# Optimization experiments

Measured on AMD Instinct MI355X. Metric: run time of the kernel, lower is better.

The kernel has to match this reference:

```python
import jax, jax.numpy as jnp
import numpy as np

B, N, E = 16, 4096, 65536
IN, H = 256, 512
G1, G2 = 32, 32
M1, M2 = 1024, 32768
GOD = 8
BN_EPS = 1e-5


def setup_inputs() -> dict:
    key = jax.random.key(0)
    ks = jax.random.split(key, 16)
    rn = lambda i, sh, s=0.05: jax.random.normal(ks[i], sh, dtype=jnp.float32) * s
    return {
        "x": jax.random.normal(ks[0], (B, IN), dtype=jnp.float32),
        "smoothed_vert_pos": jax.random.normal(ks[1], (B, N * 3), dtype=jnp.float32),
        "hidden": jnp.zeros((B, H), jnp.float32),
        "edge_index": jax.random.randint(ks[2], (2, E), 0, N),
        "W0": rn(3, (G1, 3), 0.3), "a0_src": rn(4, (G1,), 0.3), "a0_dst": rn(5, (G1,), 0.3), "b0": jnp.zeros((G1,), jnp.float32),
        "W1": rn(6, (G2, G1), 0.2), "a1_src": rn(7, (G2,), 0.2), "a1_dst": rn(8, (G2,), 0.2), "b1": jnp.zeros((G2,), jnp.float32),
        "w_ih": rn(9, (3 * H, IN)), "w_hh": rn(10, (3 * H, H)),
        "b_ih": jnp.zeros((3 * H,), jnp.float32), "b_hh": jnp.zeros((3 * H,), jnp.float32),
        "lin1_w": rn(11, (M1, H)), "lin1_b": jnp.zeros((M1,), jnp.float32),
        "prelu1": jnp.full((M1,), 0.25, jnp.float32), "bn1_g": jnp.ones((M1,), jnp.float32), "bn1_b": jnp.zeros((M1,), jnp.float32),
        "lin2_w": rn(12, (M2, M1), 0.02), "lin2_b": jnp.zeros((M2,), jnp.float32),
        "prelu2": jnp.full((M2,), 0.25, jnp.float32), "bn2_g": jnp.ones((M2,), jnp.float32), "bn2_b": jnp.zeros((M2,), jnp.float32),
        "w_out": rn(13, (3, G2 + GOD), 0.2), "b_out": jnp.zeros((3,), jnp.float32),
    }


def _gat(v, src, dst, W, a_s, a_d, b):
    # PyG GATConv, heads=1, eval mode (no dropout), self-loops already in src/dst
    h = v @ W.T                                           # [N, F]
    e = jax.nn.leaky_relu((h * a_s).sum(-1)[src] + (h * a_d).sum(-1)[dst], 0.2)  # [E+N]
    m = jax.ops.segment_max(e, dst, num_segments=N)       # segment-softmax over incoming edges
    w = jnp.exp(e - m[dst])
    s = jax.ops.segment_sum(w, dst, num_segments=N)
    coef = w / s[dst]
    return jax.ops.segment_sum(coef[:, None] * h[src], dst, num_segments=N) + b


def _mlp_layer(t, w, bb, p, g, be):
    t = t @ w.T + bb                                      # Linear
    t = jnp.where(t >= 0, t, p * t)                       # PReLU (per-channel)
    # eval BatchNorm1d with running_mean=0, running_var=1
    return (t / jnp.sqrt(1.0 + BN_EPS)) * g + be


def reference(x, smoothed_vert_pos, hidden, edge_index,
              W0, a0_src, a0_dst, b0, W1, a1_src, a1_dst, b1,
              w_ih, w_hh, b_ih, b_hh,
              lin1_w, lin1_b, prelu1, bn1_g, bn1_b,
              lin2_w, lin2_b, prelu2, bn2_g, bn2_b,
              w_out, b_out):
    sv = smoothed_vert_pos.reshape(B, N, 3)
    loop = jnp.arange(N, dtype=edge_index.dtype)
    src = jnp.concatenate([edge_index[0], loop])          # GATConv add_self_loops=True
    dst = jnp.concatenate([edge_index[1], loop])
    gat0 = jax.vmap(lambda v: _gat(v, src, dst, W0, a0_src, a0_dst, b0))(sv)   # [B,N,G1]
    gat1 = jax.vmap(lambda v: _gat(v, src, dst, W1, a1_src, a1_dst, b1))(gat0)  # [B,N,G2]

    # GRUCell
    gi = x @ w_ih.T + b_ih
    gh = hidden @ w_hh.T + b_hh
    ir, iz, inn = jnp.split(gi, 3, axis=-1)
    hr, hz, hn = jnp.split(gh, 3, axis=-1)
    r = jax.nn.sigmoid(ir + hr)
    z = jax.nn.sigmoid(iz + hz)
    n = jnp.tanh(inn + r * hn)
    next_hidden = (1.0 - z) * n + z * hidden              # [B,H]

    o = _mlp_layer(next_hidden, lin1_w, lin1_b, prelu1, bn1_g, bn1_b)
    o = _mlp_layer(o, lin2_w, lin2_b, prelu2, bn2_g, bn2_b)
    gru_out = o.reshape(B, N, GOD)

    y = (jnp.concatenate([gru_out, gat1], axis=2) @ w_out.T + b_out).reshape(B, -1)
    return y, next_hidden
```

## Files before the change

### kernel.cpp

```cpp
#include <hip/hip_runtime.h>

#define BB 16
#define NN 4096
#define EE 65536
#define HH 512
#define M1N 1024
#define M2N 32768
#define CAP 96



__global__ void k_pre(int* __restrict__ cnt,
                      const float* __restrict__ x, const float* __restrict__ hid,
                      const float* __restrict__ w_ih, const float* __restrict__ w_hh,
                      const float* __restrict__ b_ih, const float* __restrict__ b_hh,
                      float* __restrict__ nh, float* __restrict__ out_nh,
                      const float* __restrict__ svp, const float* __restrict__ W0,
                      const float* __restrict__ a0s, const float* __restrict__ a0d,
                      float* __restrict__ h0t, float* __restrict__ as0t,
                      float* __restrict__ ad0t) {
  const int bid = blockIdx.x;
  if (bid < 16) {
    cnt[bid * 256 + threadIdx.x] = 0;
    return;
  }
  if (bid < 2064) {
    int wid = (bid - 16) * 4 + (threadIdx.x >> 6);
    int lane = threadIdx.x & 63;
    int b = wid >> 9, j = wid & 511;
    const float* xb = x + b * 256;
    const float* hb = hid + b * HH;
    float ir = 0.f, iz = 0.f, in_ = 0.f, hr = 0.f, hz = 0.f, hn = 0.f;
    for (int k = lane; k < 256; k += 64) {
      float xv = xb[k];
      ir  += xv * w_ih[(size_t)j * 256 + k];
      iz  += xv * w_ih[(size_t)(j + 512) * 256 + k];
      in_ += xv * w_ih[(size_t)(j + 1024) * 256 + k];
    }
    for (int k = lane; k < 512; k += 64) {
      float hv = hb[k];
      hr += hv * w_hh[(size_t)j * 512 + k];
      hz += hv * w_hh[(size_t)(j + 512) * 512 + k];
      hn += hv * w_hh[(size_t)(j + 1024) * 512 + k];
    }
#pragma unroll
    for (int m = 1; m < 64; m <<= 1) {
      ir += __shfl_xor(ir, m, 64); iz += __shfl_xor(iz, m, 64); in_ += __shfl_xor(in_, m, 64);
      hr += __shfl_xor(hr, m, 64); hz += __shfl_xor(hz, m, 64); hn  += __shfl_xor(hn, m, 64);
    }
    if (lane == 0) {
      ir += b_ih[j]; iz += b_ih[j + 512]; in_ += b_ih[j + 1024];
      hr += b_hh[j]; hz += b_hh[j + 512]; hn += b_hh[j + 1024];
      float r = 1.f / (1.f + __expf(-(ir + hr)));
      float z = 1.f / (1.f + __expf(-(iz + hz)));
      float n = tanhf(in_ + r * hn);
      float v = (1.f - z) * n + z * hb[j];
      nh[wid] = v;
      out_nh[wid] = v;
    }
    return;
  }
  int gid = (bid - 2064) * 256 + threadIdx.x;
  int grp = gid >> 5, f = gid & 31;
  int b = grp >> 12, n = grp & 4095;
  const float* v = svp + (size_t)grp * 3;
  float hv = v[0] * W0[f * 3] + v[1] * W0[f * 3 + 1] + v[2] * W0[f * 3 + 2];
  h0t[(size_t)n * 512 + b * 32 + f] = hv;
  float ps = hv * a0s[f], pd = hv * a0d[f];
#pragma unroll
  for (int m = 1; m < 32; m <<= 1) {
    ps += __shfl_xor(ps, m, 64);
    pd += __shfl_xor(pd, m, 64);
  }
  if (f == 0) { as0t[n * 16 + b] = ps; ad0t[n * 16 + b] = pd; }
}


__global__ void k_mid1(const float* __restrict__ nh, const float* __restrict__ l1w,
                       const float* __restrict__ l1b, const float* __restrict__ p1,
                       const float* __restrict__ g1v, const float* __restrict__ be1,
                       float* __restrict__ o1,
                       const int* __restrict__ src, const int* __restrict__ dst,
                       int* __restrict__ cnt, int* __restrict__ csr) {
  const int bid = blockIdx.x;
  if (bid < 4096) {
    const int wave = threadIdx.x >> 6;
    const int lane = threadIdx.x & 63;
    int wid = bid * 4 + wave;
    int b = wid >> 10, j = wid & 1023;
    const float* hb = nh + b * HH;
    const float* wr = l1w + (size_t)j * HH;
    float acc = 0.f;
    for (int k = lane; k < HH; k += 64) acc += hb[k] * wr[k];
#pragma unroll
    for (int m = 1; m < 64; m <<= 1) acc += __shfl_xor(acc, m, 64);
    if (lane == 0) {
      float t = acc + l1b[j];
      t = t >= 0.f ? t : p1[j] * t;
      o1[wid] = t * 0.99999500003749973f * g1v[j] + be1[j];
    }
    return;
  }
  int k = (bid - 4096) * 256 + threadIdx.x;
  if (k < EE) {
    int d = dst[k];
    int slot = atomicAdd(&cnt[d], 1);
    if ((unsigned)slot < CAP) csr[d * CAP + slot] = src[k];
  }
}


__global__ __launch_bounds__(256, 4) void k_mid2(
    const float* __restrict__ o1, const float* __restrict__ l2w,
    const float* __restrict__ l2b, const float* __restrict__ p2,
    const float* __restrict__ g2v, const float* __restrict__ be2,
    float* __restrict__ o2,
    const int* __restrict__ cnt, const int* __restrict__ csr,
    const float* __restrict__ h0t, const float* __restrict__ as0t,
    const float* __restrict__ ad0t, const float* __restrict__ b0,
    const float* __restrict__ W1, const float* __restrict__ a1s,
    const float* __restrict__ a1d,
    float* __restrict__ h1t, float* __restrict__ as1t,
    float* __restrict__ ad1t) {
  const int bid = blockIdx.x;
  const int wave = threadIdx.x >> 6;
  const int lane = threadIdx.x & 63;
  __shared__ float lds[4][8][36];
  if (bid < 2048) {
    const int bh = lane >> 5;
    const int kl = lane & 31;
    const int j0 = (bid * 4 + wave) * 4;
    const float* ob = o1 + (size_t)bh * 8 * 1024;
    const float* w0 = l2w + (size_t)j0 * 1024;
    float acc[4][8];
#pragma unroll
    for (int r = 0; r < 4; r++)
#pragma unroll
      for (int b = 0; b < 8; b++) acc[r][b] = 0.f;
#pragma unroll 1
    for (int it = 0; it < 8; ++it) {
      const int kq = it * 128 + kl * 4;
      float4 wv0 = *(const float4*)(w0 + kq);
      float4 wv1 = *(const float4*)(w0 + 1024 + kq);
      float4 wv2 = *(const float4*)(w0 + 2048 + kq);
      float4 wv3 = *(const float4*)(w0 + 3072 + kq);
#pragma unroll
      for (int b = 0; b < 8; b++) {
        float4 v = *(const float4*)(ob + b * 1024 + kq);
        acc[0][b] += wv0.x*v.x + wv0.y*v.y + wv0.z*v.z + wv0.w*v.w;
        acc[1][b] += wv1.x*v.x + wv1.y*v.y + wv1.z*v.z + wv1.w*v.w;
        acc[2][b] += wv2.x*v.x + wv2.y*v.y + wv2.z*v.z + wv2.w*v.w;
        acc[3][b] += wv3.x*v.x + wv3.y*v.y + wv3.z*v.z + wv3.w*v.w;
      }
    }
#pragma unroll
    for (int r = 0; r < 4; r++)
#pragma unroll
      for (int b = 0; b < 8; b++)
#pragma unroll
        for (int m = 1; m < 32; m <<= 1)
          acc[r][b] += __shfl_xor(acc[r][b], m, 64);
    if (kl == 0) {
      const float INV = 0.99999500003749973f;
#pragma unroll
      for (int r = 0; r < 4; r++) {
        const int j = j0 + r;
        const float bj = l2b[j], pj = p2[j], gj = g2v[j], bej = be2[j];
#pragma unroll
        for (int b = 0; b < 8; b++) {
          float t = acc[r][b] + bj;
          t = t >= 0.f ? t : pj * t;
          o2[(size_t)(bh * 8 + b) * M2N + j] = t * INV * gj + bej;
        }
      }
    }
    return;
  }
  const int u  = bid - 2048;
  const int n  = u * 2 + (wave >> 1);
  const int bh = wave & 1;
  const int bl = lane >> 3;
  const int fq = lane & 7;
  const int b  = bh * 8 + bl;
  const int f0 = fq * 4;
  const int boff = b * 32 + f0;
  const int deg = min(cnt[n], CAP);
  const int base = n * CAP;
  const float adn = ad0t[n * 16 + b];
  const int total = deg + 1;
  float4 acc = {0.f, 0.f, 0.f, 0.f};
  float asum = 0.f;
  for (int i = 0; i < total; i += 4) {
    int r0 = csr[base + i];
    int r1 = csr[base + i + 1];
    int r2 = csr[base + i + 2];
    int r3 = csr[base + i + 3];
    int sv0 = (i     < deg) ? r0 : n;
    int sv1 = (i + 1 < deg) ? r1 : n;
    int sv2 = (i + 2 < deg) ? r2 : n;
    int sv3 = (i + 3 < deg) ? r3 : n;
    float e0 = as0t[sv0 * 16 + b];
    float e1 = as0t[sv1 * 16 + b];
    float e2 = as0t[sv2 * 16 + b];
    float e3 = as0t[sv3 * 16 + b];
    float4 hv0 = *(const float4*)(h0t + (size_t)sv0 * 512 + boff);
    float4 hv1 = *(const float4*)(h0t + (size_t)sv1 * 512 + boff);
    float4 hv2 = *(const float4*)(h0t + (size_t)sv2 * 512 + boff);
    float4 hv3 = *(const float4*)(h0t + (size_t)sv3 * 512 + boff);
    float e, w;
    e = e0 + adn; e = e >= 0.f ? e : 0.2f * e;
    w = (i     < total) ? __expf(e) : 0.f;
    asum += w; acc.x += w*hv0.x; acc.y += w*hv0.y; acc.z += w*hv0.z; acc.w += w*hv0.w;
    e = e1 + adn; e = e >= 0.f ? e : 0.2f * e;
    w = (i + 1 < total) ? __expf(e) : 0.f;
    asum += w; acc.x += w*hv1.x; acc.y += w*hv1.y; acc.z += w*hv1.z; acc.w += w*hv1.w;
    e = e2 + adn; e = e >= 0.f ? e : 0.2f * e;
    w = (i + 2 < total) ? __expf(e) : 0.f;
    asum += w; acc.x += w*hv2.x; acc.y += w*hv2.y; acc.z += w*hv2.z; acc.w += w*hv2.w;
    e = e3 + adn; e = e >= 0.f ? e : 0.2f * e;
    w = (i + 3 < total) ? __expf(e) : 0.f;
    asum += w; acc.x += w*hv3.x; acc.y += w*hv3.y; acc.z += w*hv3.z; acc.w += w*hv3.w;
  }
  float inv = 1.f / asum;
  float4 b0v = *(const float4*)(b0 + f0);
  float4 g0;
  g0.x = acc.x * inv + b0v.x; g0.y = acc.y * inv + b0v.y;
  g0.z = acc.z * inv + b0v.z; g0.w = acc.w * inv + b0v.w;
  *(float4*)&lds[wave][bl][f0] = g0;
  __syncthreads();
  float h1a = 0.f, h1b = 0.f, h1c = 0.f, h1d = 0.f;
  const float* gr = lds[wave][bl];
  const float* w1r = W1 + f0 * 32;
#pragma unroll
  for (int k = 0; k < 32; ++k) {
    float gk = gr[k];
    h1a += gk * w1r[k];
    h1b += gk * w1r[32 + k];
    h1c += gk * w1r[64 + k];
    h1d += gk * w1r[96 + k];
  }
  float4 h1v = {h1a, h1b, h1c, h1d};
  *(float4*)(h1t + (size_t)n * 512 + boff) = h1v;
  float ps = h1a * a1s[f0] + h1b * a1s[f0+1] + h1c * a1s[f0+2] + h1d * a1s[f0+3];
  float pd = h1a * a1d[f0] + h1b * a1d[f0+1] + h1c * a1d[f0+2] + h1d * a1d[f0+3];
#pragma unroll
  for (int m = 1; m < 8; m <<= 1) {
    ps += __shfl_xor(ps, m, 64);
    pd += __shfl_xor(pd, m, 64);
  }
  if (fq == 0) { as1t[n * 16 + b] = ps; ad1t[n * 16 + b] = pd; }
}


__global__ void k_fin(const int* __restrict__ cnt, const int* __restrict__ csr,
                      const float* __restrict__ h1t, const float* __restrict__ as1t,
                      const float* __restrict__ ad1t, const float* __restrict__ b1,
                      const float* __restrict__ o2, const float* __restrict__ wout,
                      const float* __restrict__ bout, float* __restrict__ y) {
  const int wave = threadIdx.x >> 6;
  const int lane = threadIdx.x & 63;
  const int n  = blockIdx.x * 2 + (wave >> 1);
  const int bh = wave & 1;
  const int bl = lane >> 3;
  const int fq = lane & 7;
  const int b  = bh * 8 + bl;
  const int f0 = fq * 4;
  const int boff = b * 32 + f0;
  const int deg = min(cnt[n], CAP);
  const int base = n * CAP;
  const float adn = ad1t[n * 16 + b];
  const int total = deg + 1;
  float4 acc = {0.f, 0.f, 0.f, 0.f};
  float asum = 0.f;
  for (int i = 0; i < total; i += 4) {
    int r0 = csr[base + i];
    int r1 = csr[base + i + 1];
    int r2 = csr[base + i + 2];
    int r3 = csr[base + i + 3];
    int sv0 = (i     < deg) ? r0 : n;
    int sv1 = (i + 1 < deg) ? r1 : n;
    int sv2 = (i + 2 < deg) ? r2 : n;
    int sv3 = (i + 3 < deg) ? r3 : n;
    float e0 = as1t[sv0 * 16 + b];
    float e1 = as1t[sv1 * 16 + b];
    float e2 = as1t[sv2 * 16 + b];
    float e3 = as1t[sv3 * 16 + b];
    float4 hv0 = *(const float4*)(h1t + (size_t)sv0 * 512 + boff);
    float4 hv1 = *(const float4*)(h1t + (size_t)sv1 * 512 + boff);
    float4 hv2 = *(const float4*)(h1t + (size_t)sv2 * 512 + boff);
    float4 hv3 = *(const float4*)(h1t + (size_t)sv3 * 512 + boff);
    float e, w;
    e = e0 + adn; e = e >= 0.f ? e : 0.2f * e;
    w = (i     < total) ? __expf(e) : 0.f;
    asum += w; acc.x += w*hv0.x; acc.y += w*hv0.y; acc.z += w*hv0.z; acc.w += w*hv0.w;
    e = e1 + adn; e = e >= 0.f ? e : 0.2f * e;
    w = (i + 1 < total) ? __expf(e) : 0.f;
    asum += w; acc.x += w*hv1.x; acc.y += w*hv1.y; acc.z += w*hv1.z; acc.w += w*hv1.w;
    e = e2 + adn; e = e >= 0.f ? e : 0.2f * e;
    w = (i + 2 < total) ? __expf(e) : 0.f;
    asum += w; acc.x += w*hv2.x; acc.y += w*hv2.y; acc.z += w*hv2.z; acc.w += w*hv2.w;
    e = e3 + adn; e = e >= 0.f ? e : 0.2f * e;
    w = (i + 3 < total) ? __expf(e) : 0.f;
    asum += w; acc.x += w*hv3.x; acc.y += w*hv3.y; acc.z += w*hv3.z; acc.w += w*hv3.w;
  }
  float inv = 1.f / asum;
  float4 b1v = *(const float4*)(b1 + f0);
  float gx = acc.x * inv + b1v.x, gy = acc.y * inv + b1v.y;
  float gz = acc.z * inv + b1v.z, gw = acc.w * inv + b1v.w;
  float pc0 = gx*wout[ 8+f0] + gy*wout[ 9+f0] + gz*wout[10+f0] + gw*wout[11+f0];
  float pc1 = gx*wout[48+f0] + gy*wout[49+f0] + gz*wout[50+f0] + gw*wout[51+f0];
  float pc2 = gx*wout[88+f0] + gy*wout[89+f0] + gz*wout[90+f0] + gw*wout[91+f0];
#pragma unroll
  for (int m = 1; m < 8; m <<= 1) {
    pc0 += __shfl_xor(pc0, m, 64);
    pc1 += __shfl_xor(pc1, m, 64);
    pc2 += __shfl_xor(pc2, m, 64);
  }
  if (fq == 0) {
    const float* gr = o2 + (size_t)b * M2N + n * 8;
    float4 ga = *(const float4*)gr;
    float4 gb = *(const float4*)(gr + 4);
    float c0 = pc0 + bout[0], c1 = pc1 + bout[1], c2 = pc2 + bout[2];
    c0 += ga.x*wout[0]  + ga.y*wout[1]  + ga.z*wout[2]  + ga.w*wout[3]
        + gb.x*wout[4]  + gb.y*wout[5]  + gb.z*wout[6]  + gb.w*wout[7];
    c1 += ga.x*wout[40] + ga.y*wout[41] + ga.z*wout[42] + ga.w*wout[43]
        + gb.x*wout[44] + gb.y*wout[45] + gb.z*wout[46] + gb.w*wout[47];
    c2 += ga.x*wout[80] + ga.y*wout[81] + ga.z*wout[82] + ga.w*wout[83]
        + gb.x*wout[84] + gb.y*wout[85] + gb.z*wout[86] + gb.w*wout[87];
    float* yp = y + (size_t)b * (NN * 3) + n * 3;
    yp[0] = c0; yp[1] = c1; yp[2] = c2;
  }
}


extern "C" void kernel_launch(void* const* d_in, const int* in_sizes, int n_in,
                              void* d_out, int out_size, void* d_ws, size_t ws_size,
                              hipStream_t stream) {
  const float* x    = (const float*)d_in[0];
  const float* svp  = (const float*)d_in[1];
  const float* hid  = (const float*)d_in[2];
  const int*   ei   = (const int*)d_in[3];
  const float* W0   = (const float*)d_in[4];
  const float* a0s  = (const float*)d_in[5];
  const float* a0d  = (const float*)d_in[6];
  const float* b0   = (const float*)d_in[7];
  const float* W1   = (const float*)d_in[8];
  const float* a1s  = (const float*)d_in[9];
  const float* a1d  = (const float*)d_in[10];
  const float* b1   = (const float*)d_in[11];
  const float* w_ih = (const float*)d_in[12];
  const float* w_hh = (const float*)d_in[13];
  const float* b_ih = (const float*)d_in[14];
  const float* b_hh = (const float*)d_in[15];
  const float* l1w  = (const float*)d_in[16];
  const float* l1b  = (const float*)d_in[17];
  const float* p1   = (const float*)d_in[18];
  const float* g1v  = (const float*)d_in[19];
  const float* be1  = (const float*)d_in[20];
  const float* l2w  = (const float*)d_in[21];
  const float* l2b  = (const float*)d_in[22];
  const float* p2   = (const float*)d_in[23];
  const float* g2v  = (const float*)d_in[24];
  const float* be2  = (const float*)d_in[25];
  const float* wout = (const float*)d_in[26];
  const float* bout = (const float*)d_in[27];
  float* out = (float*)d_out;

  char* ws = (char*)d_ws;
  size_t off = 0;
  auto alloc = [&](size_t bytes) -> char* {
    char* p = ws + off;
    off += (bytes + 255) & ~(size_t)255;
    return p;
  };
  int*   cnt   = (int*)alloc((size_t)NN * 4);
  int*   csr   = (int*)alloc(((size_t)NN * CAP + 16) * 4);
  float* h0t   = (float*)alloc((size_t)NN * 16 * 32 * 4);
  float* as0t  = (float*)alloc((size_t)NN * 16 * 4);
  float* ad0t  = (float*)alloc((size_t)NN * 16 * 4);
  float* h1t   = (float*)alloc((size_t)NN * 16 * 32 * 4);
  float* as1t  = (float*)alloc((size_t)NN * 16 * 4);
  float* ad1t  = (float*)alloc((size_t)NN * 16 * 4);
  float* nh    = (float*)alloc((size_t)BB * HH * 4);
  float* o1    = (float*)alloc((size_t)BB * M1N * 4);
  float* o2    = (float*)alloc((size_t)BB * M2N * 4);

  const int* srcv = ei;
  const int* dstv = ei + EE;

  k_pre<<<16 + 2048 + 8192, 256, 0, stream>>>(
      cnt, x, hid, w_ih, w_hh, b_ih, b_hh, nh, out + (size_t)BB * NN * 3,
      svp, W0, a0s, a0d, h0t, as0t, ad0t);
  k_mid1<<<4096 + 256, 256, 0, stream>>>(
      nh, l1w, l1b, p1, g1v, be1, o1, srcv, dstv, cnt, csr);
  k_mid2<<<2048 + 2048, 256, 0, stream>>>(
      o1, l2w, l2b, p2, g2v, be2, o2,
      cnt, csr, h0t, as0t, ad0t, b0, W1, a1s, a1d, h1t, as1t, ad1t);
  k_fin<<<2048, 256, 0, stream>>>(cnt, csr, h1t, as1t, ad1t, b1, o2, wout, bout, out);
}
```

Before: 127.1 us.

## Split lin2 GEMV into own kernel with LDS-staged activations and prefetch

Separates the fused lin2 GEMV and first GAT aggregation into two kernels, k_agg0 and k_lin2. The new lin2 kernel uses 512-thread blocks and stages all 64 KB of o1 activations in shared memory. It also software-prefetches the next weight chunk while computing on the current one. This is meant to cut redundant global and L2 reads of o1 and hide weight-load latency. In exchange it adds an extra launch and loses the overlap between the GEMV and the aggregation, and 64 KB of LDS per block may limit occupancy.

After: 133.5 us. 5.0% more time.

```diff
diff --git a/kernel.cpp b/kernel.cpp
--- a/kernel.cpp
+++ b/kernel.cpp
@@ -110,74 +110,17 @@
 }
 
 
-__global__ __launch_bounds__(256, 4) void k_mid2(
-    const float* __restrict__ o1, const float* __restrict__ l2w,
-    const float* __restrict__ l2b, const float* __restrict__ p2,
-    const float* __restrict__ g2v, const float* __restrict__ be2,
-    float* __restrict__ o2,
-    const int* __restrict__ cnt, const int* __restrict__ csr,
-    const float* __restrict__ h0t, const float* __restrict__ as0t,
-    const float* __restrict__ ad0t, const float* __restrict__ b0,
-    const float* __restrict__ W1, const float* __restrict__ a1s,
-    const float* __restrict__ a1d,
-    float* __restrict__ h1t, float* __restrict__ as1t,
-    float* __restrict__ ad1t) {
-  const int bid = blockIdx.x;
+__global__ void k_agg0(const int* __restrict__ cnt, const int* __restrict__ csr,
+                       const float* __restrict__ h0t, const float* __restrict__ as0t,
+                       const float* __restrict__ ad0t, const float* __restrict__ b0,
+                       const float* __restrict__ W1, const float* __restrict__ a1s,
+                       const float* __restrict__ a1d,
+                       float* __restrict__ h1t, float* __restrict__ as1t,
+                       float* __restrict__ ad1t) {
   const int wave = threadIdx.x >> 6;
   const int lane = threadIdx.x & 63;
   __shared__ float lds[4][8][36];
-  if (bid < 2048) {
-    const int bh = lane >> 5;
-    const int kl = lane & 31;
-    const int j0 = (bid * 4 + wave) * 4;
-    const float* ob = o1 + (size_t)bh * 8 * 1024;
-    const float* w0 = l2w + (size_t)j0 * 1024;
-    float acc[4][8];
-#pragma unroll
-    for (int r = 0; r < 4; r++)
-#pragma unroll
-      for (int b = 0; b < 8; b++) acc[r][b] = 0.f;
-#pragma unroll 1
-    for (int it = 0; it < 8; ++it) {
-      const int kq = it * 128 + kl * 4;
-      float4 wv0 = *(const float4*)(w0 + kq);
-      float4 wv1 = *(const float4*)(w0 + 1024 + kq);
-      float4 wv2 = *(const float4*)(w0 + 2048 + kq);
-      float4 wv3 = *(const float4*)(w0 + 3072 + kq);
-#pragma unroll
-      for (int b = 0; b < 8; b++) {
-        float4 v = *(const float4*)(ob + b * 1024 + kq);
-        acc[0][b] += wv0.x*v.x + wv0.y*v.y + wv0.z*v.z + wv0.w*v.w;
-        acc[1][b] += wv1.x*v.x + wv1.y*v.y + wv1.z*v.z + wv1.w*v.w;
-        acc[2][b] += wv2.x*v.x + wv2.y*v.y + wv2.z*v.z + wv2.w*v.w;
-        acc[3][b] += wv3.x*v.x + wv3.y*v.y + wv3.z*v.z + wv3.w*v.w;
-      }
-    }
-#pragma unroll
-    for (int r = 0; r < 4; r++)
-#pragma unroll
-      for (int b = 0; b < 8; b++)
-#pragma unroll
-        for (int m = 1; m < 32; m <<= 1)
-          acc[r][b] += __shfl_xor(acc[r][b], m, 64);
-    if (kl == 0) {
-      const float INV = 0.99999500003749973f;
-#pragma unroll
-      for (int r = 0; r < 4; r++) {
-        const int j = j0 + r;
-        const float bj = l2b[j], pj = p2[j], gj = g2v[j], bej = be2[j];
-#pragma unroll
-        for (int b = 0; b < 8; b++) {
-          float t = acc[r][b] + bj;
-          t = t >= 0.f ? t : pj * t;
-          o2[(size_t)(bh * 8 + b) * M2N + j] = t * INV * gj + bej;
-        }
-      }
-    }
-    return;
-  }
-  const int u  = bid - 2048;
-  const int n  = u * 2 + (wave >> 1);
+  const int n  = blockIdx.x * 2 + (wave >> 1);
   const int bh = wave & 1;
   const int bl = lane >> 3;
   const int fq = lane & 7;
@@ -249,6 +192,75 @@
     pd += __shfl_xor(pd, m, 64);
   }
   if (fq == 0) { as1t[n * 16 + b] = ps; ad1t[n * 16 + b] = pd; }
+}
+
+
+__global__ __launch_bounds__(512) void k_lin2(
+    const float* __restrict__ o1, const float* __restrict__ w,
+    const float* __restrict__ bias, const float* __restrict__ pr,
+    const float* __restrict__ g, const float* __restrict__ be,
+    float* __restrict__ o2) {
+  __shared__ float s_o1[16 * 1024];
+  for (int i = threadIdx.x; i < 4096; i += 512)
+    ((float4*)s_o1)[i] = ((const float4*)o1)[i];
+  __syncthreads();
+  const int wave = threadIdx.x >> 6;
+  const int lane = threadIdx.x & 63;
+  const int bh = lane >> 5;
+  const int kl = lane & 31;
+  const int j0 = blockIdx.x * 32 + wave * 4;
+  const float* w0 = w + (size_t)j0 * 1024 + kl * 4;
+  const float* ob = s_o1 + bh * 8 * 1024 + kl * 4;
+  float acc[4][8];
+#pragma unroll
+  for (int r = 0; r < 4; r++)
+#pragma unroll
+    for (int b = 0; b < 8; b++) acc[r][b] = 0.f;
+  float4 wv0 = *(const float4*)(w0);
+  float4 wv1 = *(const float4*)(w0 + 1024);
+  float4 wv2 = *(const float4*)(w0 + 2048);
+  float4 wv3 = *(const float4*)(w0 + 3072);
+#pragma unroll 1
+  for (int it = 0; it < 8; ++it) {
+    float4 cw0 = wv0, cw1 = wv1, cw2 = wv2, cw3 = wv3;
+    if (it < 7) {
+      const float* wn = w0 + (it + 1) * 128;
+      wv0 = *(const float4*)(wn);
+      wv1 = *(const float4*)(wn + 1024);
+      wv2 = *(const float4*)(wn + 2048);
+      wv3 = *(const float4*)(wn + 3072);
+    }
+    const float* oc = ob + it * 128;
+#pragma unroll
+    for (int b = 0; b < 8; b++) {
+      float4 v = *(const float4*)(oc + b * 1024);
+      acc[0][b] += cw0.x*v.x + cw0.y*v.y + cw0.z*v.z + cw0.w*v.w;
+      acc[1][b] += cw1.x*v.x + cw1.y*v.y + cw1.z*v.z + cw1.w*v.w;
+      acc[2][b] += cw2.x*v.x + cw2.y*v.y + cw2.z*v.z + cw2.w*v.w;
+      acc[3][b] += cw3.x*v.x + cw3.y*v.y + cw3.z*v.z + cw3.w*v.w;
+    }
+  }
+#pragma unroll
+  for (int r = 0; r < 4; r++)
+#pragma unroll
+    for (int b = 0; b < 8; b++)
+#pragma unroll
+      for (int m = 1; m < 32; m <<= 1)
+        acc[r][b] += __shfl_xor(acc[r][b], m, 64);
+  if (kl == 0) {
+    const float INV = 0.99999500003749973f;
+#pragma unroll
+    for (int r = 0; r < 4; r++) {
+      const int j = j0 + r;
+      const float bj = bias[j], pj = pr[j], gj = g[j], bej = be[j];
+#pragma unroll
+      for (int b = 0; b < 8; b++) {
+        float t = acc[r][b] + bj;
+        t = t >= 0.f ? t : pj * t;
+        o2[(size_t)(bh * 8 + b) * M2N + j] = t * INV * gj + bej;
+      }
+    }
+  }
 }
 
 
@@ -393,8 +405,8 @@
       svp, W0, a0s, a0d, h0t, as0t, ad0t);
   k_mid1<<<4096 + 256, 256, 0, stream>>>(
       nh, l1w, l1b, p1, g1v, be1, o1, srcv, dstv, cnt, csr);
-  k_mid2<<<2048 + 2048, 256, 0, stream>>>(
-      o1, l2w, l2b, p2, g2v, be2, o2,
+  k_agg0<<<2048, 256, 0, stream>>>(
       cnt, csr, h0t, as0t, ad0t, b0, W1, a1s, a1d, h1t, as1t, ad1t);
+  k_lin2<<<1024, 512, 0, stream>>>(o1, l2w, l2b, p2, g2v, be2, o2);
   k_fin<<<2048, 256, 0, stream>>>(cnt, csr, h1t, as1t, ad1t, b1, o2, wout, bout, out);
 }
```

## Regroup kernels: split CSR fill, pair GAT layer0 with lin1, standalone lin2

Applied to the files above, without the earlier changes.

The launch sequence is reorganised. The CSR fill now runs as its own kernel. The GAT layer-0 aggregation shares one launch with the lin1 GEMV, and the lin2 GEMV becomes a standalone kernel that computes 2 output rows per wave instead of 4, with launch bounds raised to 6. The aim is to pair work differently across kernels and to raise occupancy in the bandwidth-bound lin2 weight stream. The cost is one extra kernel launch, and in the lin2 kernel the o1 activation vector is reloaded more often.

Measured after the change: 140.1 us. 10.2% more time.

```diff
diff --git a/kernel.cpp b/kernel.cpp
--- a/kernel.cpp
+++ b/kernel.cpp
@@ -76,32 +76,9 @@
 }
 
 
-__global__ void k_mid1(const float* __restrict__ nh, const float* __restrict__ l1w,
-                       const float* __restrict__ l1b, const float* __restrict__ p1,
-                       const float* __restrict__ g1v, const float* __restrict__ be1,
-                       float* __restrict__ o1,
-                       const int* __restrict__ src, const int* __restrict__ dst,
-                       int* __restrict__ cnt, int* __restrict__ csr) {
-  const int bid = blockIdx.x;
-  if (bid < 4096) {
-    const int wave = threadIdx.x >> 6;
-    const int lane = threadIdx.x & 63;
-    int wid = bid * 4 + wave;
-    int b = wid >> 10, j = wid & 1023;
-    const float* hb = nh + b * HH;
-    const float* wr = l1w + (size_t)j * HH;
-    float acc = 0.f;
-    for (int k = lane; k < HH; k += 64) acc += hb[k] * wr[k];
-#pragma unroll
-    for (int m = 1; m < 64; m <<= 1) acc += __shfl_xor(acc, m, 64);
-    if (lane == 0) {
-      float t = acc + l1b[j];
-      t = t >= 0.f ? t : p1[j] * t;
-      o1[wid] = t * 0.99999500003749973f * g1v[j] + be1[j];
-    }
-    return;
-  }
-  int k = (bid - 4096) * 256 + threadIdx.x;
+__global__ void k_fill2(const int* __restrict__ src, const int* __restrict__ dst,
+                        int* __restrict__ cnt, int* __restrict__ csr) {
+  int k = blockIdx.x * 256 + threadIdx.x;
   if (k < EE) {
     int d = dst[k];
     int slot = atomicAdd(&cnt[d], 1);
@@ -110,145 +87,162 @@
 }
 
 
-__global__ __launch_bounds__(256, 4) void k_mid2(
-    const float* __restrict__ o1, const float* __restrict__ l2w,
-    const float* __restrict__ l2b, const float* __restrict__ p2,
-    const float* __restrict__ g2v, const float* __restrict__ be2,
-    float* __restrict__ o2,
-    const int* __restrict__ cnt, const int* __restrict__ csr,
-    const float* __restrict__ h0t, const float* __restrict__ as0t,
-    const float* __restrict__ ad0t, const float* __restrict__ b0,
-    const float* __restrict__ W1, const float* __restrict__ a1s,
-    const float* __restrict__ a1d,
-    float* __restrict__ h1t, float* __restrict__ as1t,
-    float* __restrict__ ad1t) {
+__global__ void k_mid(const int* __restrict__ cnt, const int* __restrict__ csr,
+                      const float* __restrict__ h0t, const float* __restrict__ as0t,
+                      const float* __restrict__ ad0t, const float* __restrict__ b0,
+                      const float* __restrict__ W1, const float* __restrict__ a1s,
+                      const float* __restrict__ a1d,
+                      float* __restrict__ h1t, float* __restrict__ as1t,
+                      float* __restrict__ ad1t,
+                      const float* __restrict__ nh, const float* __restrict__ l1w,
+                      const float* __restrict__ l1b, const float* __restrict__ p1,
+                      const float* __restrict__ g1v, const float* __restrict__ be1,
+                      float* __restrict__ o1) {
   const int bid = blockIdx.x;
   const int wave = threadIdx.x >> 6;
   const int lane = threadIdx.x & 63;
-  __shared__ float lds[4][8][36];
   if (bid < 2048) {
-    const int bh = lane >> 5;
-    const int kl = lane & 31;
-    const int j0 = (bid * 4 + wave) * 4;
-    const float* ob = o1 + (size_t)bh * 8 * 1024;
-    const float* w0 = l2w + (size_t)j0 * 1024;
-    float acc[4][8];
-#pragma unroll
-    for (int r = 0; r < 4; r++)
-#pragma unroll
-      for (int b = 0; b < 8; b++) acc[r][b] = 0.f;
+    __shared__ float lds[4][8][36];
+    const int n  = bid * 2 + (wave >> 1);
+    const int bh = wave & 1;
+    const int bl = lane >> 3;
+    const int fq = lane & 7;
+    const int b  = bh * 8 + bl;
+    const int f0 = fq * 4;
+    const int boff = b * 32 + f0;
+    const int deg = min(cnt[n], CAP);
+    const int base = n * CAP;
+    const float adn = ad0t[n * 16 + b];
+    const int total = deg + 1;
+    float4 acc = {0.f, 0.f, 0.f, 0.f};
+    float asum = 0.f;
+    for (int i = 0; i < total; i += 4) {
+      int r0 = csr[base + i];
+      int r1 = csr[base + i + 1];
+      int r2 = csr[base + i + 2];
+      int r3 = csr[base + i + 3];
+      int sv0 = (i     < deg) ? r0 : n;
+      int sv1 = (i + 1 < deg) ? r1 : n;
+      int sv2 = (i + 2 < deg) ? r2 : n;
+      int sv3 = (i + 3 < deg) ? r3 : n;
+      float e0 = as0t[sv0 * 16 + b];
+      float e1 = as0t[sv1 * 16 + b];
+      float e2 = as0t[sv2 * 16 + b];
+      float e3 = as0t[sv3 * 16 + b];
+      float4 hv0 = *(const float4*)(h0t + (size_t)sv0 * 512 + boff);
+      float4 hv1 = *(const float4*)(h0t + (size_t)sv1 * 512 + boff);
+      float4 hv2 = *(const float4*)(h0t + (size_t)sv2 * 512 + boff);
+      float4 hv3 = *(const float4*)(h0t + (size_t)sv3 * 512 + boff);
+      float e, w;
+      e = e0 + adn; e = e >= 0.f ? e : 0.2f * e;
+      w = (i     < total) ? __expf(e) : 0.f;
+      asum += w; acc.x += w*hv0.x; acc.y += w*hv0.y; acc.z += w*hv0.z; acc.w += w*hv0.w;
+      e = e1 + adn; e = e >= 0.f ? e : 0.2f * e;
+      w = (i + 1 < total) ? __expf(e) : 0.f;
+      asum += w; acc.x += w*hv1.x; acc.y += w*hv1.y; acc.z += w*hv1.z; acc.w += w*hv1.w;
+      e = e2 + adn; e = e >= 0.f ? e : 0.2f * e;
+      w = (i + 2 < total) ? __expf(e) : 0.f;
+      asum += w; acc.x += w*hv2.x; acc.y += w*hv2.y; acc.z += w*hv2.z; acc.w += w*hv2.w;
+      e = e3 + adn; e = e >= 0.f ? e : 0.2f * e;
+      w = (i + 3 < total) ? __expf(e) : 0.f;
+      asum += w; acc.x += w*hv3.x; acc.y += w*hv3.y; acc.z += w*hv3.z; acc.w += w*hv3.w;
+    }
+    float inv = 1.f / asum;
+    float4 b0v = *(const float4*)(b0 + f0);
+    float4 g0;
+    g0.x = acc.x * inv + b0v.x; g0.y = acc.y * inv + b0v.y;
+    g0.z = acc.z * inv + b0v.z; g0.w = acc.w * inv + b0v.w;
+    *(float4*)&lds[wave][bl][f0] = g0;
+    __syncthreads();
+    float h1a = 0.f, h1b = 0.f, h1c = 0.f, h1d = 0.f;
+    const float* gr = lds[wave][bl];
+    const float* w1r = W1 + f0 * 32;
+#pragma unroll
+    for (int k = 0; k < 32; ++k) {
+      float gk = gr[k];
+      h1a += gk * w1r[k];
+      h1b += gk * w1r[32 + k];
+      h1c += gk * w1r[64 + k];
+      h1d += gk * w1r[96 + k];
+    }
+    float4 h1v = {h1a, h1b, h1c, h1d};
+    *(float4*)(h1t + (size_t)n * 512 + boff) = h1v;
+    float ps = h1a * a1s[f0] + h1b * a1s[f0+1] + h1c * a1s[f0+2] + h1d * a1s[f0+3];
+    float pd = h1a * a1d[f0] + h1b * a1d[f0+1] + h1c * a1d[f0+2] + h1d * a1d[f0+3];
+#pragma unroll
+    for (int m = 1; m < 8; m <<= 1) {
+      ps += __shfl_xor(ps, m, 64);
+      pd += __shfl_xor(pd, m, 64);
+    }
+    if (fq == 0) { as1t[n * 16 + b] = ps; ad1t[n * 16 + b] = pd; }
+    return;
+  }
+  int wid = (bid - 2048) * 4 + wave;
+  int b = wid >> 10, j = wid & 1023;
+  const float* hb = nh + b * HH;
+  const float* wr = l1w + (size_t)j * HH;
+  float acc = 0.f;
+  for (int k = lane; k < HH; k += 64) acc += hb[k] * wr[k];
+#pragma unroll
+  for (int m = 1; m < 64; m <<= 1) acc += __shfl_xor(acc, m, 64);
+  if (lane == 0) {
+    float t = acc + l1b[j];
+    t = t >= 0.f ? t : p1[j] * t;
+    o1[wid] = t * 0.99999500003749973f * g1v[j] + be1[j];
+  }
+}
+
+
+__global__ __launch_bounds__(256, 6) void k_lin2(
+    const float* __restrict__ o1, const float* __restrict__ w,
+    const float* __restrict__ bias, const float* __restrict__ pr,
+    const float* __restrict__ g, const float* __restrict__ be,
+    float* __restrict__ o2) {
+  const int wave = threadIdx.x >> 6;
+  const int lane = threadIdx.x & 63;
+  const int bh = lane >> 5;
+  const int kl = lane & 31;
+  const int j0 = (blockIdx.x * 4 + wave) * 2;
+  const float* ob = o1 + (size_t)bh * 8 * 1024;
+  const float* w0 = w + (size_t)j0 * 1024;
+  float acc[2][8];
+#pragma unroll
+  for (int r = 0; r < 2; r++)
+#pragma unroll
+    for (int b = 0; b < 8; b++) acc[r][b] = 0.f;
 #pragma unroll 1
-    for (int it = 0; it < 8; ++it) {
-      const int kq = it * 128 + kl * 4;
-      float4 wv0 = *(const float4*)(w0 + kq);
-      float4 wv1 = *(const float4*)(w0 + 1024 + kq);
-      float4 wv2 = *(const float4*)(w0 + 2048 + kq);
-      float4 wv3 = *(const float4*)(w0 + 3072 + kq);
+  for (int it = 0; it < 8; ++it) {
+    const int kq = it * 128 + kl * 4;
+    float4 wv0 = *(const float4*)(w0 + kq);
+    float4 wv1 = *(const float4*)(w0 + 1024 + kq);
+#pragma unroll
+    for (int b = 0; b < 8; b++) {
+      float4 v = *(const float4*)(ob + b * 1024 + kq);
+      acc[0][b] += wv0.x*v.x + wv0.y*v.y + wv0.z*v.z + wv0.w*v.w;
+      acc[1][b] += wv1.x*v.x + wv1.y*v.y + wv1.z*v.z + wv1.w*v.w;
+    }
+  }
+#pragma unroll
+  for (int r = 0; r < 2; r++)
+#pragma unroll
+    for (int b = 0; b < 8; b++)
+#pragma unroll
+      for (int m = 1; m < 32; m <<= 1)
+        acc[r][b] += __shfl_xor(acc[r][b], m, 64);
+  if (kl == 0) {
+    const float INV = 0.99999500003749973f;
+#pragma unroll
+    for (int r = 0; r < 2; r++) {
+      const int j = j0 + r;
+      const float bj = bias[j], pj = pr[j], gj = g[j], bej = be[j];
 #pragma unroll
       for (int b = 0; b < 8; b++) {
-        float4 v = *(const float4*)(ob + b * 1024 + kq);
-        acc[0][b] += wv0.x*v.x + wv0.y*v.y + wv0.z*v.z + wv0.w*v.w;
-        acc[1][b] += wv1.x*v.x + wv1.y*v.y + wv1.z*v.z + wv1.w*v.w;
-        acc[2][b] += wv2.x*v.x + wv2.y*v.y + wv2.z*v.z + wv2.w*v.w;
-        acc[3][b] += wv3.x*v.x + wv3.y*v.y + wv3.z*v.z + wv3.w*v.w;
+        float t = acc[r][b] + bj;
+        t = t >= 0.f ? t : pj * t;
+        o2[(size_t)(bh * 8 + b) * M2N + j] = t * INV * gj + bej;
       }
     }
-#pragma unroll
-    for (int r = 0; r < 4; r++)
-#pragma unroll
-      for (int b = 0; b < 8; b++)
-#pragma unroll
-        for (int m = 1; m < 32; m <<= 1)
-          acc[r][b] += __shfl_xor(acc[r][b], m, 64);
-    if (kl == 0) {
-      const float INV = 0.99999500003749973f;
-#pragma unroll
-      for (int r = 0; r < 4; r++) {
-        const int j = j0 + r;
-        const float bj = l2b[j], pj = p2[j], gj = g2v[j], bej = be2[j];
-#pragma unroll
-        for (int b = 0; b < 8; b++) {
-          float t = acc[r][b] + bj;
-          t = t >= 0.f ? t : pj * t;
-          o2[(size_t)(bh * 8 + b) * M2N + j] = t * INV * gj + bej;
-        }
-      }
-    }
-    return;
-  }
-  const int u  = bid - 2048;
-  const int n  = u * 2 + (wave >> 1);
-  const int bh = wave & 1;
-  const int bl = lane >> 3;
-  const int fq = lane & 7;
-  const int b  = bh * 8 + bl;
-  const int f0 = fq * 4;
-  const int boff = b * 32 + f0;
-  const int deg = min(cnt[n], CAP);
-  const int base = n * CAP;
-  const float adn = ad0t[n * 16 + b];
-  const int total = deg + 1;
-  float4 acc = {0.f, 0.f, 0.f, 0.f};
-  float asum = 0.f;
-  for (int i = 0; i < total; i += 4) {
-    int r0 = csr[base + i];
-    int r1 = csr[base + i + 1];
-    int r2 = csr[base + i + 2];
-    int r3 = csr[base + i + 3];
-    int sv0 = (i     < deg) ? r0 : n;
-    int sv1 = (i + 1 < deg) ? r1 : n;
-    int sv2 = (i + 2 < deg) ? r2 : n;
-    int sv3 = (i + 3 < deg) ? r3 : n;
-    float e0 = as0t[sv0 * 16 + b];
-    float e1 = as0t[sv1 * 16 + b];
-    float e2 = as0t[sv2 * 16 + b];
-    float e3 = as0t[sv3 * 16 + b];
-    float4 hv0 = *(const float4*)(h0t + (size_t)sv0 * 512 + boff);
-    float4 hv1 = *(const float4*)(h0t + (size_t)sv1 * 512 + boff);
-    float4 hv2 = *(const float4*)(h0t + (size_t)sv2 * 512 + boff);
-    float4 hv3 = *(const float4*)(h0t + (size_t)sv3 * 512 + boff);
-    float e, w;
-    e = e0 + adn; e = e >= 0.f ? e : 0.2f * e;
-    w = (i     < total) ? __expf(e) : 0.f;
-    asum += w; acc.x += w*hv0.x; acc.y += w*hv0.y; acc.z += w*hv0.z; acc.w += w*hv0.w;
-    e = e1 + adn; e = e >= 0.f ? e : 0.2f * e;
-    w = (i + 1 < total) ? __expf(e) : 0.f;
-    asum += w; acc.x += w*hv1.x; acc.y += w*hv1.y; acc.z += w*hv1.z; acc.w += w*hv1.w;
-    e = e2 + adn; e = e >= 0.f ? e : 0.2f * e;
-    w = (i + 2 < total) ? __expf(e) : 0.f;
-    asum += w; acc.x += w*hv2.x; acc.y += w*hv2.y; acc.z += w*hv2.z; acc.w += w*hv2.w;
-    e = e3 + adn; e = e >= 0.f ? e : 0.2f * e;
-    w = (i + 3 < total) ? __expf(e) : 0.f;
-    asum += w; acc.x += w*hv3.x; acc.y += w*hv3.y; acc.z += w*hv3.z; acc.w += w*hv3.w;
-  }
-  float inv = 1.f / asum;
-  float4 b0v = *(const float4*)(b0 + f0);
-  float4 g0;
-  g0.x = acc.x * inv + b0v.x; g0.y = acc.y * inv + b0v.y;
-  g0.z = acc.z * inv + b0v.z; g0.w = acc.w * inv + b0v.w;
-  *(float4*)&lds[wave][bl][f0] = g0;
-  __syncthreads();
-  float h1a = 0.f, h1b = 0.f, h1c = 0.f, h1d = 0.f;
-  const float* gr = lds[wave][bl];
-  const float* w1r = W1 + f0 * 32;
-#pragma unroll
-  for (int k = 0; k < 32; ++k) {
-    float gk = gr[k];
-    h1a += gk * w1r[k];
-    h1b += gk * w1r[32 + k];
-    h1c += gk * w1r[64 + k];
-    h1d += gk * w1r[96 + k];
-  }
-  float4 h1v = {h1a, h1b, h1c, h1d};
-  *(float4*)(h1t + (size_t)n * 512 + boff) = h1v;
-  float ps = h1a * a1s[f0] + h1b * a1s[f0+1] + h1c * a1s[f0+2] + h1d * a1s[f0+3];
-  float pd = h1a * a1d[f0] + h1b * a1d[f0+1] + h1c * a1d[f0+2] + h1d * a1d[f0+3];
-#pragma unroll
-  for (int m = 1; m < 8; m <<= 1) {
-    ps += __shfl_xor(ps, m, 64);
-    pd += __shfl_xor(pd, m, 64);
-  }
-  if (fq == 0) { as1t[n * 16 + b] = ps; ad1t[n * 16 + b] = pd; }
+  }
 }
 
 
@@ -391,10 +385,10 @@
   k_pre<<<16 + 2048 + 8192, 256, 0, stream>>>(
       cnt, x, hid, w_ih, w_hh, b_ih, b_hh, nh, out + (size_t)BB * NN * 3,
       svp, W0, a0s, a0d, h0t, as0t, ad0t);
-  k_mid1<<<4096 + 256, 256, 0, stream>>>(
-      nh, l1w, l1b, p1, g1v, be1, o1, srcv, dstv, cnt, csr);
-  k_mid2<<<2048 + 2048, 256, 0, stream>>>(
-      o1, l2w, l2b, p2, g2v, be2, o2,
-      cnt, csr, h0t, as0t, ad0t, b0, W1, a1s, a1d, h1t, as1t, ad1t);
+  k_fill2<<<EE / 256, 256, 0, stream>>>(srcv, dstv, cnt, csr);
+  k_mid<<<2048 + 4096, 256, 0, stream>>>(
+      cnt, csr, h0t, as0t, ad0t, b0, W1, a1s, a1d, h1t, as1t, ad1t,
+      nh, l1w, l1b, p1, g1v, be1, o1);
+  k_lin2<<<M2N / 8, 256, 0, stream>>>(o1, l2w, l2b, p2, g2v, be2, o2);
   k_fin<<<2048, 256, 0, stream>>>(cnt, csr, h1t, as1t, ad1t, b1, o2, wout, bout, out);
 }
```
